# Performance work log

Measured on AMD Instinct MI355X. Metric: run time of the kernel, lower is better.

The kernel has to match this reference:

```python
import jax, jax.numpy as jnp
import numpy as np

E, T, IN, OUT, GS = 8, 2048, 2048, 2048, 64


def setup_inputs() -> dict:
    key = jax.random.key(0)
    k1, k2, k3, k4, k5 = jax.random.split(key, 5)
    x = jax.random.normal(k1, (T, IN), dtype=jnp.float32)
    # int4 codes in [0,16): stored unpacked as int32 for the reference
    qweight = jax.random.randint(k2, (E, IN, OUT), 0, 16, dtype=jnp.int32)
    G = IN // GS  # quant groups along the reduction dim
    scales = jax.random.uniform(k3, (E, G, OUT), jnp.float32, minval=0.005, maxval=0.02)
    zeros = jax.random.normal(k4, (E, G, OUT), jnp.float32) * 0.01
    scales_and_zeros = jnp.stack([scales, zeros], axis=-1)  # [E, G, OUT, 2]
    # tokens sorted by expert: per-expert counts are diffs of sorted cut points, sum == T
    cuts = jnp.sort(jax.random.randint(k5, (E - 1,), 0, T + 1, dtype=jnp.int32))
    bounds = jnp.concatenate([jnp.zeros((1,), jnp.int32), cuts, jnp.full((1,), T, jnp.int32)])
    tokens_per_expert = jnp.diff(bounds).astype(jnp.int32)  # [E]
    return {
        "x": x,
        "qweight": qweight,
        "scales_and_zeros": scales_and_zeros,
        "tokens_per_expert": tokens_per_expert,
        "group_size": GS,
    }


def reference(x, qweight, scales_and_zeros, tokens_per_expert, group_size):
    """Grouped (per-expert) int4 dequant + GEMM over an expert-sorted token matrix.

    Math of aten._weight_int4pack_mm per expert e over each quant group g:
        W_e[k, n] = (q_e[k, n] - 8) * scale_e[g, n] + zero_e[g, n],  g = k // group_size
        out[rows_e] = x[rows_e] @ W_e
    where rows_e is the contiguous slice given by cumsum(tokens_per_expert).
    """
    n_exp, in_f, out_f = qweight.shape
    n_tok = x.shape[0]
    G = in_f // group_size

    # dequantize all expert weights: [E, IN, OUT]
    q = qweight.reshape(n_exp, G, group_size, out_f).astype(x.dtype)
    scales = scales_and_zeros[..., 0][:, :, None, :]  # [E, G, 1, OUT]
    zeros = scales_and_zeros[..., 1][:, :, None, :]   # [E, G, 1, OUT]
    W = ((q - 8.0) * scales + zeros).reshape(n_exp, in_f, out_f)

    # expert id per token from the cumsum boundaries (tokens are expert-sorted)
    cum = jnp.cumsum(tokens_per_expert)                                # [E]
    eid = jnp.searchsorted(cum, jnp.arange(n_tok), side="right")       # [T]
    onehot = (eid[:, None] == jnp.arange(n_exp)[None, :]).astype(x.dtype)  # [T, E]

    # dispatch -> per-expert GEMM -> combine (jit-safe grouped GEMM)
    xe = jnp.einsum("te,ti->eti", onehot, x)       # [E, T, IN]
    ye = jnp.einsum("eti,eio->eto", xe, W)         # [E, T, OUT]
    out = jnp.einsum("te,eto->to", onehot, ye)     # [T, OUT]
    return out
```

## Files before the change

kernel.cpp:

```cpp
#include <hip/hip_runtime.h>
#include <hip/hip_bf16.h>

constexpr int NE  = 8;
constexpr int T   = 2048;
constexpr int IN  = 2048;
constexpr int OUT = 2048;
constexpr int GS  = 64;
constexpr int G   = IN / GS;

constexpr int BN = 64;
constexpr int KC = 512;
constexpr int KSPLIT = IN / KC;
constexpr int LDB = KC + 8;

using short8  = __attribute__((ext_vector_type(8))) short;
using floatx4 = __attribute__((ext_vector_type(4))) float;

__global__ __launch_bounds__(256)
void cvt_x_bf16(const float* __restrict__ x, __hip_bfloat16* __restrict__ xb) {
    const int i = (blockIdx.x * 256 + threadIdx.x) * 4;
    const float4 v = *(const float4*)(x + i);
    union { unsigned long long u; __hip_bfloat162 h2[2]; } p;
    p.h2[0] = __float22bfloat162_rn(float2{v.x, v.y});
    p.h2[1] = __float22bfloat162_rn(float2{v.z, v.w});
    *(unsigned long long*)(xb + i) = p.u;
}

__global__ __launch_bounds__(256, 2)
void hqq_grouped_gemm(const __hip_bfloat16* __restrict__ xb,
                      const int*   __restrict__ qw,
                      const float* __restrict__ snz,
                      const int*   __restrict__ tpe,
                      float* __restrict__ out) {
    const int tid = threadIdx.x;
    const int e   = blockIdx.z;
    const int kc  = blockIdx.y * KC;
    const int n0  = blockIdx.x * BN;

    int b0 = 0;
    for (int i = 0; i < NE; ++i) {
        int c = tpe[i];
        if (i < e) b0 += c;
    }
    const int b1 = b0 + tpe[e];
    const int nrows = b1 - b0;
    if (nrows <= 0) return;

    __shared__ __hip_bfloat16 Bs[BN][LDB];

    const int bn_ = tid & 63;
    const int ko  = (tid >> 6) * 8;
    const int*    qcol  = qw + (size_t)e * IN * OUT + (size_t)kc * OUT + n0 + bn_;
    const float2* szcol = (const float2*)snz + (size_t)e * G * OUT + n0 + bn_;

#pragma unroll 4
    for (int i = 0; i < 16; ++i) {
        const int kb = ko + 32 * i;
        const int g  = (kc + kb) >> 6;
        const float2 sz = szcol[(size_t)g * OUT];
        const float s = sz.x;
        const float c = sz.y - 8.0f * s;
        const int* qp = qcol + (size_t)kb * OUT;
        int q[8];
#pragma unroll
        for (int j = 0; j < 8; ++j)
            q[j] = qp[(size_t)j * OUT];
        union { short8 v; __hip_bfloat162 h2[4]; } pb;
#pragma unroll
        for (int j = 0; j < 4; ++j) {
            const float f0 = (float)q[2 * j]     * s + c;
            const float f1 = (float)q[2 * j + 1] * s + c;
            pb.h2[j] = __float22bfloat162_rn(float2{f0, f1});
        }
        *(short8*)&Bs[bn_][kb] = pb.v;
    }

    __syncthreads();

    const int lane = tid & 63;
    const int wid  = tid >> 6;
    const int lm = lane & 15;
    const int lk = (lane >> 4) * 8;
    const int lq = (lane >> 4) * 4;

    for (int mt = wid; mt * 32 < nrows; mt += 4) {
        const int r0 = b0 + mt * 32;

        const __hip_bfloat16* abase[2];
#pragma unroll
        for (int i = 0; i < 2; ++i) {
            const int row = r0 + i * 16 + lm;
            const int rr  = row < b1 ? row : (b1 - 1);
            abase[i] = xb + (size_t)rr * IN + kc + lk;
        }

        floatx4 acc[2][4];
#pragma unroll
        for (int i = 0; i < 2; ++i)
#pragma unroll
            for (int j = 0; j < 4; ++j)
                acc[i][j] = (floatx4){0.f, 0.f, 0.f, 0.f};

#pragma unroll 4
        for (int ks = 0; ks < KC; ks += 32) {
            short8 af[2], bfr[4];
#pragma unroll
            for (int i = 0; i < 2; ++i)
                af[i] = *(const short8*)(abase[i] + ks);
#pragma unroll
            for (int j = 0; j < 4; ++j)
                bfr[j] = *(const short8*)&Bs[j * 16 + lm][ks + lk];
#pragma unroll
            for (int i = 0; i < 2; ++i)
#pragma unroll
                for (int j = 0; j < 4; ++j)
                    acc[i][j] = __builtin_amdgcn_mfma_f32_16x16x32_bf16(
                        af[i], bfr[j], acc[i][j], 0, 0, 0);
        }

#pragma unroll
        for (int i = 0; i < 2; ++i) {
#pragma unroll
            for (int r = 0; r < 4; ++r) {
                const int row = r0 + i * 16 + lq + r;
                if (row < b1) {
                    float* op = out + (size_t)row * OUT + n0 + lm;
#pragma unroll
                    for (int j = 0; j < 4; ++j)
                        atomicAdd(op + j * 16, acc[i][j][r]);
                }
            }
        }
    }
}

extern "C" void kernel_launch(void* const* d_in, const int* in_sizes, int n_in,
                              void* d_out, int out_size, void* d_ws, size_t ws_size,
                              hipStream_t stream) {
    const float* x   = (const float*)d_in[0];
    const int*   qw  = (const int*)d_in[1];
    const float* snz = (const float*)d_in[2];
    const int*   tpe = (const int*)d_in[3];
    float* out = (float*)d_out;
    __hip_bfloat16* xb = (__hip_bfloat16*)d_ws;

    hipMemsetAsync(out, 0, (size_t)out_size * sizeof(float), stream);

    cvt_x_bf16<<<(T * IN) / (256 * 4), 256, 0, stream>>>(x, xb);

    dim3 grid(OUT / BN, KSPLIT, NE);
    hqq_grouped_gemm<<<grid, 256, 0, stream>>>(xb, qw, snz, tpe, out);
}
```

Before: 271.6 us.

## Replace split-K atomics with partial buffers and reduction; double-buffer A loads

When the workspace is large enough, each K-split writes its partial tile to its own buffer with plain stores, and a separate kernel sums the four partials into the output. This replaces the memset and the float atomicAdds. The A-fragment loads in the MFMA loop are also software-pipelined over two register buffers of 128-wide K chunks, and the dequant loop unroll goes from 4 to 8. The cost is extra global traffic for writing and rereading the partial buffers (4x the output size), one more launch, and higher register pressure. If the workspace is too small, the old atomic path still runs.

New measurement: 309.5 us. 14.0% more time.

```diff
diff --git a/kernel.cpp b/kernel.cpp
--- a/kernel.cpp
+++ b/kernel.cpp
@@ -26,15 +26,29 @@
     *(unsigned long long*)(xb + i) = p.u;
 }
 
+__global__ __launch_bounds__(256)
+void reduce_part(const float* __restrict__ part, float* __restrict__ out) {
+    const size_t i = ((size_t)blockIdx.x * 256 + threadIdx.x) * 4;
+    float4 s = *(const float4*)(part + i);
+#pragma unroll
+    for (int p = 1; p < KSPLIT; ++p) {
+        const float4 v = *(const float4*)(part + (size_t)p * T * OUT + i);
+        s.x += v.x; s.y += v.y; s.z += v.z; s.w += v.w;
+    }
+    *(float4*)(out + i) = s;
+}
+
+template <bool ATOMIC>
 __global__ __launch_bounds__(256, 2)
 void hqq_grouped_gemm(const __hip_bfloat16* __restrict__ xb,
                       const int*   __restrict__ qw,
                       const float* __restrict__ snz,
                       const int*   __restrict__ tpe,
-                      float* __restrict__ out) {
+                      float* __restrict__ outp) {
     const int tid = threadIdx.x;
     const int e   = blockIdx.z;
-    const int kc  = blockIdx.y * KC;
+    const int kci = blockIdx.y;
+    const int kc  = kci * KC;
     const int n0  = blockIdx.x * BN;
 
     int b0 = 0;
@@ -53,7 +67,7 @@
     const int*    qcol  = qw + (size_t)e * IN * OUT + (size_t)kc * OUT + n0 + bn_;
     const float2* szcol = (const float2*)snz + (size_t)e * G * OUT + n0 + bn_;
 
-#pragma unroll 4
+#pragma unroll 8
     for (int i = 0; i < 16; ++i) {
         const int kb = ko + 32 * i;
         const int g  = (kc + kb) >> 6;
@@ -83,6 +97,8 @@
     const int lk = (lane >> 4) * 8;
     const int lq = (lane >> 4) * 4;
 
+    float* const obase = ATOMIC ? outp : outp + (size_t)kci * T * OUT;
+
     for (int mt = wid; mt * 32 < nrows; mt += 4) {
         const int r0 = b0 + mt * 32;
 
@@ -101,22 +117,36 @@
             for (int j = 0; j < 4; ++j)
                 acc[i][j] = (floatx4){0.f, 0.f, 0.f, 0.f};
 
-#pragma unroll 4
-        for (int ks = 0; ks < KC; ks += 32) {
-            short8 af[2], bfr[4];
+        short8 bufA[8], bufB[8];
+        auto loadc = [&](short8* buf, int c) {
+            const int ksb = c * 128;
 #pragma unroll
-            for (int i = 0; i < 2; ++i)
-                af[i] = *(const short8*)(abase[i] + ks);
+            for (int s = 0; s < 4; ++s)
 #pragma unroll
-            for (int j = 0; j < 4; ++j)
-                bfr[j] = *(const short8*)&Bs[j * 16 + lm][ks + lk];
+                for (int i = 0; i < 2; ++i)
+                    buf[s * 2 + i] = *(const short8*)(abase[i] + ksb + s * 32);
+        };
+        auto mfmac = [&](short8* buf, int c) {
+            const int ksb = c * 128;
 #pragma unroll
-            for (int i = 0; i < 2; ++i)
+            for (int s = 0; s < 4; ++s) {
+                short8 bfr[4];
 #pragma unroll
                 for (int j = 0; j < 4; ++j)
-                    acc[i][j] = __builtin_amdgcn_mfma_f32_16x16x32_bf16(
-                        af[i], bfr[j], acc[i][j], 0, 0, 0);
-        }
+                    bfr[j] = *(const short8*)&Bs[j * 16 + lm][ksb + s * 32 + lk];
+#pragma unroll
+                for (int i = 0; i < 2; ++i)
+#pragma unroll
+                    for (int j = 0; j < 4; ++j)
+                        acc[i][j] = __builtin_amdgcn_mfma_f32_16x16x32_bf16(
+                            buf[s * 2 + i], bfr[j], acc[i][j], 0, 0, 0);
+            }
+        };
+        loadc(bufA, 0); loadc(bufB, 1);
+        mfmac(bufA, 0); loadc(bufA, 2);
+        mfmac(bufB, 1); loadc(bufB, 3);
+        mfmac(bufA, 2);
+        mfmac(bufB, 3);
 
 #pragma unroll
         for (int i = 0; i < 2; ++i) {
@@ -124,10 +154,12 @@
             for (int r = 0; r < 4; ++r) {
                 const int row = r0 + i * 16 + lq + r;
                 if (row < b1) {
-                    float* op = out + (size_t)row * OUT + n0 + lm;
+                    float* op = obase + (size_t)row * OUT + n0 + lm;
 #pragma unroll
-                    for (int j = 0; j < 4; ++j)
-                        atomicAdd(op + j * 16, acc[i][j][r]);
+                    for (int j = 0; j < 4; ++j) {
+                        if (ATOMIC) atomicAdd(op + j * 16, acc[i][j][r]);
+                        else        op[j * 16] = acc[i][j][r];
+                    }
                 }
             }
         }
@@ -142,12 +174,21 @@
     const float* snz = (const float*)d_in[2];
     const int*   tpe = (const int*)d_in[3];
     float* out = (float*)d_out;
+
+    const size_t xb_bytes   = (size_t)T * IN * sizeof(__hip_bfloat16);
+    const size_t part_bytes = (size_t)KSPLIT * T * OUT * sizeof(float);
+
     __hip_bfloat16* xb = (__hip_bfloat16*)d_ws;
-
-    hipMemsetAsync(out, 0, (size_t)out_size * sizeof(float), stream);
-
     cvt_x_bf16<<<(T * IN) / (256 * 4), 256, 0, stream>>>(x, xb);
 
     dim3 grid(OUT / BN, KSPLIT, NE);
-    hqq_grouped_gemm<<<grid, 256, 0, stream>>>(xb, qw, snz, tpe, out);
+
+    if (ws_size >= xb_bytes + part_bytes) {
+        float* part = (float*)((char*)d_ws + xb_bytes);
+        hqq_grouped_gemm<false><<<grid, 256, 0, stream>>>(xb, qw, snz, tpe, part);
+        reduce_part<<<(T * OUT) / (256 * 4), 256, 0, stream>>>(part, out);
+    } else {
+        hipMemsetAsync(out, 0, (size_t)out_size * sizeof(float), stream);
+        hqq_grouped_gemm<true><<<grid, 256, 0, stream>>>(xb, qw, snz, tpe, out);
+    }
 }
```
